# Kernel tuning notes

Hardware: AMD Instinct MI355X
Metric: run time of the kernel (lower is better)

## Reference

```python
import jax, jax.numpy as jnp
import numpy as np
import math

H = 512
V = 64
N = 128
L = 256
T = 20  # min(max_letters, word_tensor.shape[-1])


def _lstm_cell(x, h, c, Wih, Whh, bih, bhh):
    # PyTorch gate order: i, f, g, o
    gates = x @ Wih.T + h @ Whh.T + bih + bhh  # (N, 4H)
    i, f, g, o = jnp.split(gates, 4, axis=-1)
    c_new = jax.nn.sigmoid(f) * c + jax.nn.sigmoid(i) * jnp.tanh(g)
    h_new = jax.nn.sigmoid(o) * jnp.tanh(c_new)
    return h_new, c_new


def setup_inputs() -> dict:
    k = jax.random.key(0)
    ks = jax.random.split(k, 16)
    s = 0.05  # keep activations in a sane range
    return {
        "key": jax.random.normal(ks[0], (N, L, H), jnp.float32),
        "value": jax.random.normal(ks[1], (N, L, H), jnp.float32),
        "encoder_hidden": jax.random.normal(ks[2], (2, N, H), jnp.float32),
        "encoder_cell": jax.random.normal(ks[3], (2, N, H), jnp.float32),
        "word_tensor": jax.random.randint(ks[4], (N, T), 0, V, jnp.int64),
        "embedding": jax.random.normal(ks[5], (V, H), jnp.float32) * s,
        "W_ih0": jax.random.normal(ks[6], (4 * H, 2 * H), jnp.float32) * s,
        "W_hh0": jax.random.normal(ks[7], (4 * H, H), jnp.float32) * s,
        "b_ih0": jax.random.normal(ks[8], (4 * H,), jnp.float32) * s,
        "b_hh0": jax.random.normal(ks[9], (4 * H,), jnp.float32) * s,
        "W_ih1": jax.random.normal(ks[10], (4 * H, H), jnp.float32) * s,
        "W_hh1": jax.random.normal(ks[11], (4 * H, H), jnp.float32) * s,
        "b_ih1": jax.random.normal(ks[12], (4 * H,), jnp.float32) * s,
        "b_hh1": jax.random.normal(ks[13], (4 * H,), jnp.float32) * s,
        "fc_w": jax.random.normal(ks[14], (V, H), jnp.float32) * s,
        "fc_b": jax.random.normal(ks[15], (V,), jnp.float32) * s,
    }


def reference(key, value, encoder_hidden, encoder_cell, word_tensor,
              embedding, W_ih0, W_hh0, b_ih0, b_hh0,
              W_ih1, W_hh1, b_ih1, b_hh1, fc_w, fc_b):
    scale = 1.0 / math.sqrt(H)
    # force_ratio=1.0 -> always teacher-force: inputs are [SOS=0, word[:, :-1]]
    tokens = jnp.concatenate(
        [jnp.zeros((word_tensor.shape[0], 1), word_tensor.dtype),
         word_tensor[:, : T - 1]], axis=1)  # (N, T)
    tokens_t = tokens.T  # (T, N)

    def step(carry, tok):
        h, c = carry  # each (2, N, H)
        emb = embedding[tok]  # (N, H)
        q = h[-1]  # query from top-layer hidden, (N, H)
        scores = jnp.einsum('nh,nlh->nl', q, key) * scale
        attn = jax.nn.softmax(scores, axis=-1)
        ctx = jnp.einsum('nl,nlh->nh', attn, value)  # (N, H)
        x = jnp.concatenate([emb, ctx], axis=-1)  # (N, 2H)
        h0, c0 = _lstm_cell(x, h[0], c[0], W_ih0, W_hh0, b_ih0, b_hh0)
        h1, c1 = _lstm_cell(h0, h[1], c[1], W_ih1, W_hh1, b_ih1, b_hh1)
        logits = h1 @ fc_w.T + fc_b  # (N, V)
        return (jnp.stack([h0, h1]), jnp.stack([c0, c1])), logits

    (h_fin, c_fin), logits_t = jax.lax.scan(step, (encoder_hidden, encoder_cell), tokens_t)
    logits = jnp.transpose(logits_t, (1, 0, 2))  # (N, T, V)
    probs = jax.nn.softmax(logits, axis=-1)
    return probs, h_fin, c_fin
```

## Files before the change

kernel.cpp:

```cpp
#include <hip/hip_runtime.h>
#include <math.h>


#define HH 512
#define VV 64
#define NN 128
#define LL 256
#define TT 20
#define FH 2048
#define LKP 136
#define CSP 36

typedef __attribute__((ext_vector_type(8))) short bf16x8;
typedef __attribute__((ext_vector_type(4))) float f32x4;

__device__ __forceinline__ float sigf(float x) { return 1.0f / (1.0f + expf(-x)); }

__device__ __forceinline__ float wred_max(float x) {
#pragma unroll
  for (int o = 32; o > 0; o >>= 1) x = fmaxf(x, __shfl_xor(x, o));
  return x;
}
__device__ __forceinline__ float wred_sum(float x) {
#pragma unroll
  for (int o = 32; o > 0; o >>= 1) x += __shfl_xor(x, o);
  return x;
}

__global__ __launch_bounds__(256) void k_init(const float* __restrict__ eh,
                                              const float* __restrict__ ec,
                                              float* __restrict__ h0,
                                              float* __restrict__ h1,
                                              float* __restrict__ cfin) {
  int i = blockIdx.x * 256 + threadIdx.x;
  const int NH4 = NN * HH / 4;
  float4 v = ((const float4*)eh)[i];
  if (i < NH4) ((float4*)h0)[i] = v;
  else         ((float4*)h1)[i - NH4] = v;
  ((float4*)cfin)[i] = ((const float4*)ec)[i];
}

__global__ __launch_bounds__(256) void k_pre(const float* __restrict__ emb,
                                             const float* __restrict__ Wih0,
                                             const float* __restrict__ bih0,
                                             const float* __restrict__ bhh0,
                                             float* __restrict__ G) {
  int v = threadIdx.x & 63, jj = threadIdx.x >> 6;
  int j = blockIdx.x * 4 + jj;
  const float4* e4 = (const float4*)(emb + (size_t)v * HH);
  const float4* w4 = (const float4*)(Wih0 + (size_t)j * (2 * HH));
  float acc = 0.f;
#pragma unroll 8
  for (int k = 0; k < HH / 4; ++k) {
    float4 a = e4[k], b = w4[k];
    acc += a.x * b.x + a.y * b.y + a.z * b.z + a.w * b.w;
  }
  G[(size_t)v * FH + ((j & 511) << 2) + (j >> 9)] = acc + bih0[j] + bhh0[j];
}

template <bool DO_FC>
__global__ __launch_bounds__(256) void k_attn2(
    const float* __restrict__ key, const float* __restrict__ value,
    const float* __restrict__ h1cur,
    const float* __restrict__ fc_w, const float* __restrict__ fc_b,
    float* __restrict__ probs, int tprev,
    float* __restrict__ ctxp, float* __restrict__ ms) {
  __shared__ float qs[HH];
  __shared__ float scp[2][128];
  __shared__ float att[128];
  __shared__ float lg[VV];
  __shared__ float red[4];
  int b = blockIdx.x, n = b >> 1, half = b & 1, tid = threadIdx.x;
  ((float2*)qs)[tid] = ((const float2*)(h1cur + (size_t)n * HH))[tid];
  __syncthreads();

  if (DO_FC && half == 0) {
    int v = tid >> 2, p = tid & 3;
    const float4* wr = (const float4*)(fc_w + (size_t)v * HH + p * 128);
    const float4* q4 = (const float4*)(qs + p * 128);
    float a = 0.f;
#pragma unroll 8
    for (int k = 0; k < 32; ++k) {
      float4 w = wr[k], q = q4[k];
      a += w.x * q.x + w.y * q.y + w.z * q.z + w.w * q.w;
    }
    a += __shfl_xor(a, 1);
    a += __shfl_xor(a, 2);
    if (p == 0) lg[v] = a + fc_b[v];
    __syncthreads();
    if (tid < VV) {
      float x = lg[tid];
      float m = wred_max(x);
      float e = expf(x - m);
      float s = wred_sum(e);
      probs[((size_t)n * TT + tprev) * VV + tid] = e / s;
    }
  }

  const float SCALE = 0.044194173824159216f;
  int ll = tid & 127, p = tid >> 7;
  {
    const float4* kr =
        (const float4*)(key + ((size_t)n * LL + half * 128 + ll) * HH + p * 256);
    const float4* q4 = (const float4*)(qs + p * 256);
    float a = 0.f;
#pragma unroll 8
    for (int k = 0; k < 64; ++k) {
      float4 w = kr[k], q = q4[k];
      a += w.x * q.x + w.y * q.y + w.z * q.z + w.w * q.w;
    }
    scp[p][ll] = a;
  }
  __syncthreads();

  float x = 0.f;
  if (tid < 128) {
    x = (scp[0][tid] + scp[1][tid]) * SCALE;
    float m = wred_max(x);
    if ((tid & 63) == 0) red[tid >> 6] = m;
  }
  __syncthreads();
  float m_p = fmaxf(red[0], red[1]);
  if (tid < 128) {
    float e = expf(x - m_p);
    att[tid] = e;
    float s = wred_sum(e);
    if ((tid & 63) == 0) red[2 + (tid >> 6)] = s;
  }
  __syncthreads();
  if (tid == 0) {
    float2 v2 = {m_p, red[2] + red[3]};
    *(float2*)(ms + ((size_t)half * NN + n) * 2) = v2;
  }

  const float* vb = value + ((size_t)n * LL + half * 128) * HH + 2 * tid;
  float cx = 0.f, cy = 0.f;
#pragma unroll 4
  for (int l2 = 0; l2 < 128; ++l2) {
    float a2 = att[l2];
    float2 v2 = *(const float2*)(vb + (size_t)l2 * HH);
    cx += a2 * v2.x;
    cy += a2 * v2.y;
  }
  float2 o2 = {cx, cy};
  ((float2*)(ctxp + ((size_t)half * NN + n) * HH))[tid] = o2;
}

__global__ __launch_bounds__(256) void k_final(
    const float* __restrict__ h1cur, const float* __restrict__ h0cur,
    const float* __restrict__ fc_w, const float* __restrict__ fc_b,
    float* __restrict__ probs, float* __restrict__ hfin) {
  __shared__ float qs[HH];
  __shared__ float lg[VV];
  int n = blockIdx.x, tid = threadIdx.x;
  ((float2*)qs)[tid] = ((const float2*)(h1cur + (size_t)n * HH))[tid];
  ((float2*)(hfin + (size_t)n * HH))[tid] =
      ((const float2*)(h0cur + (size_t)n * HH))[tid];
  ((float2*)(hfin + (size_t)(NN + n) * HH))[tid] =
      ((const float2*)(h1cur + (size_t)n * HH))[tid];
  __syncthreads();
  int v = tid >> 2, p = tid & 3;
  const float4* wr = (const float4*)(fc_w + (size_t)v * HH + p * 128);
  const float4* q4 = (const float4*)(qs + p * 128);
  float a = 0.f;
#pragma unroll 8
  for (int k = 0; k < 32; ++k) {
    float4 w = wr[k], q = q4[k];
    a += w.x * q.x + w.y * q.y + w.z * q.z + w.w * q.w;
  }
  a += __shfl_xor(a, 1);
  a += __shfl_xor(a, 2);
  if (p == 0) lg[v] = a + fc_b[v];
  __syncthreads();
  if (tid < VV) {
    float x = lg[tid];
    float m = wred_max(x);
    float e = expf(x - m);
    float s = wred_sum(e);
    probs[((size_t)n * TT + TT - 1) * VV + tid] = e / s;
  }
}

template <int COMBINE>
__global__ __launch_bounds__(256) void k_gemm(
    const float* __restrict__ Ax0, const float* __restrict__ Ax1,
    const float* __restrict__ Ahh,
    const float* __restrict__ W0, int ws0,
    const float* __restrict__ W1, int ws1,
    const int* __restrict__ word, const float* __restrict__ G,
    const float* __restrict__ bih, const float* __restrict__ bhh,
    const float* __restrict__ ms,
    float* __restrict__ cbuf, float* __restrict__ hnext, int t) {
  __shared__ __align__(16) unsigned short AhS[32 * LKP];
  __shared__ __align__(16) unsigned short AlS[32 * LKP];
  __shared__ __align__(16) unsigned short WhS[32 * LKP];
  __shared__ __align__(16) unsigned short WlS[32 * LKP];
  __shared__ float sc0s[32], sc1s[32];
  __shared__ __align__(16) float Cs[32 * CSP];

  int tid = threadIdx.x;
  int mt = blockIdx.x & 3, nt = blockIdx.x >> 2;
  int s0 = mt * 32, n0 = nt * 32;

  int r = tid >> 3, kq = tid & 7, kk = kq * 16;
  int rowp = n0 + r;
  int jrow = (rowp & 3) * 512 + (rowp >> 2);

  if (COMBINE && tid < 32) {
    int n = s0 + tid;
    float m0 = ms[2 * n], sa = ms[2 * n + 1];
    float m1 = ms[2 * (NN + n)], sb = ms[2 * (NN + n) + 1];
    float m = fmaxf(m0, m1);
    float e0 = expf(m0 - m), e1 = expf(m1 - m);
    float S = sa * e0 + sb * e1;
    sc0s[tid] = e0 / S;
    sc1s[tid] = e1 / S;
  }

  float4 aR0[4], aR1[4], wRg[4];

  auto LOADC = [&](int c) {
    int k0 = c * 128;
    if (k0 < 512) {
      const float4* p0 = (const float4*)(Ax0 + (size_t)(s0 + r) * HH + k0 + kk);
#pragma unroll
      for (int i = 0; i < 4; ++i) aR0[i] = p0[i];
      if (COMBINE) {
        const float4* p1 = (const float4*)(Ax1 + (size_t)(s0 + r) * HH + k0 + kk);
#pragma unroll
        for (int i = 0; i < 4; ++i) aR1[i] = p1[i];
      }
      const float4* wp = (const float4*)(W0 + (size_t)jrow * ws0 + k0 + kk);
#pragma unroll
      for (int i = 0; i < 4; ++i) wRg[i] = wp[i];
    } else {
      const float4* p0 =
          (const float4*)(Ahh + (size_t)(s0 + r) * HH + (k0 - 512) + kk);
#pragma unroll
      for (int i = 0; i < 4; ++i) aR0[i] = p0[i];
      const float4* wp = (const float4*)(W1 + (size_t)jrow * ws1 + (k0 - 512) + kk);
#pragma unroll
      for (int i = 0; i < 4; ++i) wRg[i] = wp[i];
    }
  };

  auto STOREC = [&](int c) {
    int k0 = c * 128;
    bool cmb = COMBINE && (k0 < 512);
    float sa = cmb ? sc0s[r] : 0.f, sb = cmb ? sc1s[r] : 0.f;
#pragma unroll
    for (int i = 0; i < 2; ++i) {
      float xa[8], xw[8];
      float4 u0 = aR0[2 * i], u1 = aR0[2 * i + 1];
      xa[0] = u0.x; xa[1] = u0.y; xa[2] = u0.z; xa[3] = u0.w;
      xa[4] = u1.x; xa[5] = u1.y; xa[6] = u1.z; xa[7] = u1.w;
      if (cmb) {
        float4 v0 = aR1[2 * i], v1 = aR1[2 * i + 1];
        xa[0] = sa * xa[0] + sb * v0.x; xa[1] = sa * xa[1] + sb * v0.y;
        xa[2] = sa * xa[2] + sb * v0.z; xa[3] = sa * xa[3] + sb * v0.w;
        xa[4] = sa * xa[4] + sb * v1.x; xa[5] = sa * xa[5] + sb * v1.y;
        xa[6] = sa * xa[6] + sb * v1.z; xa[7] = sa * xa[7] + sb * v1.w;
      }
      float4 w0 = wRg[2 * i], w1 = wRg[2 * i + 1];
      xw[0] = w0.x; xw[1] = w0.y; xw[2] = w0.z; xw[3] = w0.w;
      xw[4] = w1.x; xw[5] = w1.y; xw[6] = w1.z; xw[7] = w1.w;
      bf16x8 ah, al, wh, wl;
#pragma unroll
      for (int j = 0; j < 8; ++j) {
        unsigned int u = __float_as_uint(xa[j]);
        unsigned int hb = (u + 0x7FFFu + ((u >> 16) & 1u)) & 0xFFFF0000u;
        ah[j] = (short)(hb >> 16);
        float lo = xa[j] - __uint_as_float(hb);
        unsigned int ul = __float_as_uint(lo);
        al[j] = (short)((ul + 0x7FFFu + ((ul >> 16) & 1u)) >> 16);
        u = __float_as_uint(xw[j]);
        hb = (u + 0x7FFFu + ((u >> 16) & 1u)) & 0xFFFF0000u;
        wh[j] = (short)(hb >> 16);
        lo = xw[j] - __uint_as_float(hb);
        ul = __float_as_uint(lo);
        wl[j] = (short)((ul + 0x7FFFu + ((ul >> 16) & 1u)) >> 16);
      }
      int off = r * LKP + kk + i * 8;
      *(bf16x8*)(AhS + off) = ah;
      *(bf16x8*)(AlS + off) = al;
      *(bf16x8*)(WhS + off) = wh;
      *(bf16x8*)(WlS + off) = wl;
    }
  };

  f32x4 acc0 = {0.f, 0.f, 0.f, 0.f};
  f32x4 acc1 = {0.f, 0.f, 0.f, 0.f};
  f32x4 acc2 = {0.f, 0.f, 0.f, 0.f};
  int lane = tid & 63, wv = tid >> 6;
  int wm = wv >> 1, wn = wv & 1;
  int aoff = (wm * 16 + (lane & 15)) * LKP;
  int woff = (wn * 16 + (lane & 15)) * LKP;
  int kb = (lane >> 4) * 8;

  LOADC(0);
  __syncthreads();
  for (int c = 0; c < 8; ++c) {
    if (c) __syncthreads();
    STOREC(c);
    __syncthreads();
    if (c < 7) LOADC(c + 1);
#pragma unroll
    for (int ks = 0; ks < 4; ++ks) {
      int ko = kb + ks * 32;
      bf16x8 ah = *(const bf16x8*)(AhS + aoff + ko);
      bf16x8 al = *(const bf16x8*)(AlS + aoff + ko);
      bf16x8 wh = *(const bf16x8*)(WhS + woff + ko);
      bf16x8 wl = *(const bf16x8*)(WlS + woff + ko);
      acc0 = __builtin_amdgcn_mfma_f32_16x16x32_bf16(ah, wh, acc0, 0, 0, 0);
      acc1 = __builtin_amdgcn_mfma_f32_16x16x32_bf16(al, wh, acc1, 0, 0, 0);
      acc2 = __builtin_amdgcn_mfma_f32_16x16x32_bf16(ah, wl, acc2, 0, 0, 0);
    }
  }

  __syncthreads();
  f32x4 cv = acc0 + acc1;
  cv = cv + acc2;
  int crow = wm * 16 + (lane >> 4) * 4, ccol = wn * 16 + (lane & 15);
#pragma unroll
  for (int q = 0; q < 4; ++q) Cs[(crow + q) * CSP + ccol] = cv[q];
  __syncthreads();
  int s_l = tid >> 3, jh_l = tid & 7;
  int s = s0 + s_l, jh = nt * 8 + jh_l;
  f32x4 c4 = *(const f32x4*)(Cs + s_l * CSP + jh_l * 4);
  if (COMBINE) {
    int tok = (t == 0) ? 0 : (word[s * TT + t - 1] & 63);
    f32x4 g4 = *(const f32x4*)(G + (size_t)tok * FH + jh * 4);
    c4 = c4 + g4;
  } else {
    c4[0] += bih[jh] + bhh[jh];
    c4[1] += bih[512 + jh] + bhh[512 + jh];
    c4[2] += bih[1024 + jh] + bhh[1024 + jh];
    c4[3] += bih[1536 + jh] + bhh[1536 + jh];
  }
  float c_old = cbuf[(size_t)s * HH + jh];
  float cn = sigf(c4[1]) * c_old + sigf(c4[0]) * tanhf(c4[2]);
  cbuf[(size_t)s * HH + jh] = cn;
  hnext[(size_t)s * HH + jh] = sigf(c4[3]) * tanhf(cn);
}

extern "C" void kernel_launch(void* const* d_in, const int* in_sizes, int n_in,
                              void* d_out, int out_size, void* d_ws, size_t ws_size,
                              hipStream_t stream) {
  const float* key   = (const float*)d_in[0];
  const float* value = (const float*)d_in[1];
  const float* eh    = (const float*)d_in[2];
  const float* ec    = (const float*)d_in[3];
  const int*   word  = (const int*)d_in[4];
  const float* emb   = (const float*)d_in[5];
  const float* Wih0  = (const float*)d_in[6];
  const float* Whh0  = (const float*)d_in[7];
  const float* bih0  = (const float*)d_in[8];
  const float* bhh0  = (const float*)d_in[9];
  const float* Wih1  = (const float*)d_in[10];
  const float* Whh1  = (const float*)d_in[11];
  const float* bih1  = (const float*)d_in[12];
  const float* bhh1  = (const float*)d_in[13];
  const float* fcw   = (const float*)d_in[14];
  const float* fcb   = (const float*)d_in[15];

  float* out   = (float*)d_out;
  float* probs = out;
  float* hfin  = out + (size_t)NN * TT * VV;
  float* cfin  = hfin + 2 * (size_t)NN * HH;

  float* ws   = (float*)d_ws;
  float* G    = ws;
  float* ctxp = G + (size_t)VV * FH;
  float* ms   = ctxp + 2 * (size_t)NN * HH;
  float* h0a  = ms + 2 * (size_t)NN * 2;
  float* h0b  = h0a + (size_t)NN * HH;
  float* h1a  = h0b + (size_t)NN * HH;
  float* h1b  = h1a + (size_t)NN * HH;

  k_init<<<128, 256, 0, stream>>>(eh, ec, h0a, h1a, cfin);
  k_pre<<<512, 256, 0, stream>>>(emb, Wih0, bih0, bhh0, G);

  float* h0c = h0a; float* h0n = h0b;
  float* h1c = h1a; float* h1n = h1b;

  for (int t = 0; t < TT; ++t) {
    if (t == 0)
      k_attn2<false><<<256, 256, 0, stream>>>(key, value, h1c, fcw, fcb,
                                              probs, 0, ctxp, ms);
    else
      k_attn2<true><<<256, 256, 0, stream>>>(key, value, h1c, fcw, fcb,
                                             probs, t - 1, ctxp, ms);

    k_gemm<1><<<256, 256, 0, stream>>>(
        ctxp, ctxp + (size_t)NN * HH, h0c, Wih0 + 512, 2 * HH, Whh0, HH,
        word, G, bih0, bhh0, ms, cfin, h0n, t);
    k_gemm<0><<<256, 256, 0, stream>>>(
        h0n, (const float*)nullptr, h1c, Wih1, HH, Whh1, HH,
        word, G, bih1, bhh1, ms, cfin + (size_t)NN * HH, h1n, t);

    float* tmp;
    tmp = h0c; h0c = h0n; h0n = tmp;
    tmp = h1c; h1c = h1n; h1n = tmp;
  }

  k_final<<<128, 256, 0, stream>>>(h1c, h0c, fcw, fcb, probs, hfin);
}
```

Before: 1.310 ms.

## Convert key/value to bf16 once and split attention into score and context kernels

Adds one-time kernels that convert key to bf16 and value to a transposed bf16 layout. Each step's attention then becomes two kernels: a score kernel with per-32-chunk softmax partials, and a context kernel that merges the partials and reads the transposed value. This halves the per-step key/value bytes, which are read 20 times, and raises block count for parallelism. The cost is an extra launch per step, bf16 rounding error in the attention, and an upfront conversion pass; the old path is kept as a fallback when the workspace is too small.

```diff
diff --git a/kernel.cpp b/kernel.cpp
--- a/kernel.cpp
+++ b/kernel.cpp
@@ -15,6 +15,13 @@
 typedef __attribute__((ext_vector_type(4))) float f32x4;
 
 __device__ __forceinline__ float sigf(float x) { return 1.0f / (1.0f + expf(-x)); }
+__device__ __forceinline__ unsigned short f2bf(float x) {
+  unsigned int u = __float_as_uint(x);
+  return (unsigned short)((u + 0x7FFFu + ((u >> 16) & 1u)) >> 16);
+}
+__device__ __forceinline__ float bf2f(short b) {
+  return __uint_as_float(((unsigned int)(unsigned short)b) << 16);
+}
 
 __device__ __forceinline__ float wred_max(float x) {
 #pragma unroll
@@ -26,6 +33,7 @@
   for (int o = 32; o > 0; o >>= 1) x += __shfl_xor(x, o);
   return x;
 }
+
 
 __global__ __launch_bounds__(256) void k_init(const float* __restrict__ eh,
                                               const float* __restrict__ ec,
@@ -58,6 +66,216 @@
   G[(size_t)v * FH + ((j & 511) << 2) + (j >> 9)] = acc + bih0[j] + bhh0[j];
 }
 
+__global__ __launch_bounds__(256) void k_prepK(const float* __restrict__ K,
+                                               unsigned short* __restrict__ Kb) {
+  size_t i = ((size_t)blockIdx.x * 256 + threadIdx.x) * 8;
+  float4 a = *(const float4*)(K + i);
+  float4 b = *(const float4*)(K + i + 4);
+  bf16x8 o;
+  o[0] = f2bf(a.x); o[1] = f2bf(a.y); o[2] = f2bf(a.z); o[3] = f2bf(a.w);
+  o[4] = f2bf(b.x); o[5] = f2bf(b.y); o[6] = f2bf(b.z); o[7] = f2bf(b.w);
+  *(bf16x8*)(Kb + i) = o;
+}
+
+__global__ __launch_bounds__(256) void k_prepVt(const float* __restrict__ V,
+                                                unsigned short* __restrict__ Vt) {
+  __shared__ float tile[64 * 65];
+  int bx = blockIdx.x;
+  int n = bx >> 5, lt = (bx >> 3) & 3, ht = bx & 7;
+  int l0 = lt * 64, h0 = ht * 64;
+  int tid = threadIdx.x;
+  int r = tid >> 2, c = (tid & 3) * 16;
+  const float4* src = (const float4*)(V + ((size_t)n * LL + l0 + r) * HH + h0 + c);
+#pragma unroll
+  for (int j = 0; j < 4; ++j) {
+    float4 u = src[j];
+    tile[r * 65 + c + j * 4 + 0] = u.x;
+    tile[r * 65 + c + j * 4 + 1] = u.y;
+    tile[r * 65 + c + j * 4 + 2] = u.z;
+    tile[r * 65 + c + j * 4 + 3] = u.w;
+  }
+  __syncthreads();
+  int hrow = tid >> 2, lcol = (tid & 3) * 16;
+  bf16x8 o0, o1;
+#pragma unroll
+  for (int j = 0; j < 8; ++j) o0[j] = f2bf(tile[(lcol + j) * 65 + hrow]);
+#pragma unroll
+  for (int j = 0; j < 8; ++j) o1[j] = f2bf(tile[(lcol + 8 + j) * 65 + hrow]);
+  bf16x8* dst = (bf16x8*)(Vt + ((size_t)n * HH + h0 + hrow) * LL + l0 + lcol);
+  dst[0] = o0;
+  dst[1] = o1;
+}
+
+
+#define ASCALE 0.044194173824159216f
+
+__global__ __launch_bounds__(256) void k_score(
+    const unsigned short* __restrict__ Kb, const float* __restrict__ h1cur,
+    float* __restrict__ sc, float* __restrict__ msb) {
+  __shared__ float qs[HH];
+  __shared__ float srow[32];
+  int bx = blockIdx.x, tid = threadIdx.x;
+  int n = bx >> 3, lq = bx & 7;
+  ((float2*)qs)[tid] = ((const float2*)(h1cur + (size_t)n * HH))[tid];
+  __syncthreads();
+  int row = tid >> 3, p = tid & 7;
+  const bf16x8* kr =
+      (const bf16x8*)(Kb + ((size_t)n * LL + lq * 32 + row) * HH + p * 64);
+  float a = 0.f;
+#pragma unroll
+  for (int i = 0; i < 8; ++i) {
+    bf16x8 kv = kr[i];
+    const float* q8 = qs + p * 64 + i * 8;
+#pragma unroll
+    for (int j = 0; j < 8; ++j) a += bf2f(kv[j]) * q8[j];
+  }
+  a += __shfl_xor(a, 1);
+  a += __shfl_xor(a, 2);
+  a += __shfl_xor(a, 4);
+  if (p == 0) srow[row] = a * ASCALE;
+  __syncthreads();
+  if (tid < 32) {
+    float x = srow[tid];
+    float m = x;
+#pragma unroll
+    for (int o = 16; o > 0; o >>= 1) m = fmaxf(m, __shfl_xor(m, o));
+    float e = expf(x - m);
+    float s = e;
+#pragma unroll
+    for (int o = 16; o > 0; o >>= 1) s += __shfl_xor(s, o);
+    sc[(size_t)n * LL + lq * 32 + tid] = e;
+    if (tid == 0) {
+      float2 v2 = {m, s};
+      *(float2*)(msb + ((size_t)lq * NN + n) * 2) = v2;
+    }
+  }
+}
+
+template <bool DO_FC>
+__global__ __launch_bounds__(256) void k_ctx(
+    const unsigned short* __restrict__ Vt, const float* __restrict__ sc,
+    const float* __restrict__ msb, float* __restrict__ ctx,
+    const float* __restrict__ h1cur, const float* __restrict__ fc_w,
+    const float* __restrict__ fc_b, float* __restrict__ probs, int tprev) {
+  __shared__ float att[LL];
+  __shared__ float redP[128];
+  __shared__ float hs[8 * HH];
+  int bx = blockIdx.x, tid = threadIdx.x;
+
+  if (DO_FC && bx >= 512) {
+    int n0 = (bx - 512) * 8;
+#pragma unroll
+    for (int i = 0; i < 4; ++i) {
+      int fi = tid + i * 256;
+      int r = fi >> 7, k4 = fi & 127;
+      ((float4*)hs)[r * 128 + k4] =
+          ((const float4*)(h1cur + (size_t)(n0 + r) * HH))[k4];
+    }
+    __syncthreads();
+    int nl = tid >> 5, vb = (tid & 31) * 2;
+    const float4* h4 = (const float4*)(hs + nl * HH);
+    const float4* w0 = (const float4*)(fc_w + (size_t)vb * HH);
+    const float4* w1 = (const float4*)(fc_w + (size_t)(vb + 1) * HH);
+    float a0 = 0.f, a1 = 0.f;
+#pragma unroll 8
+    for (int k = 0; k < 128; ++k) {
+      float4 h = h4[k], x0 = w0[k], x1 = w1[k];
+      a0 += h.x * x0.x + h.y * x0.y + h.z * x0.z + h.w * x0.w;
+      a1 += h.x * x1.x + h.y * x1.y + h.z * x1.z + h.w * x1.w;
+    }
+    a0 += fc_b[vb];
+    a1 += fc_b[vb + 1];
+    float m = fmaxf(a0, a1);
+#pragma unroll
+    for (int o = 16; o > 0; o >>= 1) m = fmaxf(m, __shfl_xor(m, o));
+    float e0 = expf(a0 - m), e1 = expf(a1 - m);
+    float s = e0 + e1;
+#pragma unroll
+    for (int o = 16; o > 0; o >>= 1) s += __shfl_xor(s, o);
+    float inv = 1.f / s;
+    float2 pr = {e0 * inv, e1 * inv};
+    *(float2*)(probs + ((size_t)(n0 + nl) * TT + tprev) * VV + vb) = pr;
+    return;
+  }
+
+  int n = bx >> 2, ht = bx & 3;
+  int hl = tid & 127, lg = tid >> 7;
+  float mp[8], sp[8];
+#pragma unroll
+  for (int i = 0; i < 8; ++i) {
+    float2 v2 = *(const float2*)(msb + ((size_t)i * NN + n) * 2);
+    mp[i] = v2.x;
+    sp[i] = v2.y;
+  }
+  float m = mp[0];
+#pragma unroll
+  for (int i = 1; i < 8; ++i) m = fmaxf(m, mp[i]);
+  float S = 0.f;
+#pragma unroll
+  for (int i = 0; i < 8; ++i) {
+    mp[i] = expf(mp[i] - m);
+    S += sp[i] * mp[i];
+  }
+  float invS = 1.f / S;
+  {
+    int l = tid;
+    att[l] = sc[(size_t)n * LL + l] * mp[l >> 5] * invS;
+  }
+  __syncthreads();
+
+  int h = ht * 128 + hl;
+  const bf16x8* vt =
+      (const bf16x8*)(Vt + ((size_t)n * HH + h) * LL + lg * 128);
+  const float* ab = att + lg * 128;
+  float acc = 0.f;
+#pragma unroll
+  for (int i = 0; i < 16; ++i) {
+    bf16x8 v8 = vt[i];
+    const float* a8 = ab + i * 8;
+#pragma unroll
+    for (int j = 0; j < 8; ++j) acc += bf2f(v8[j]) * a8[j];
+  }
+  if (lg == 1) redP[hl] = acc;
+  __syncthreads();
+  if (lg == 0) ctx[(size_t)n * HH + h] = acc + redP[hl];
+}
+
+__global__ __launch_bounds__(256) void k_final(
+    const float* __restrict__ h1cur, const float* __restrict__ h0cur,
+    const float* __restrict__ fc_w, const float* __restrict__ fc_b,
+    float* __restrict__ probs, float* __restrict__ hfin) {
+  __shared__ float qs[HH];
+  __shared__ float lg[VV];
+  int n = blockIdx.x, tid = threadIdx.x;
+  ((float2*)qs)[tid] = ((const float2*)(h1cur + (size_t)n * HH))[tid];
+  ((float2*)(hfin + (size_t)n * HH))[tid] =
+      ((const float2*)(h0cur + (size_t)n * HH))[tid];
+  ((float2*)(hfin + (size_t)(NN + n) * HH))[tid] =
+      ((const float2*)(h1cur + (size_t)n * HH))[tid];
+  __syncthreads();
+  int v = tid >> 2, p = tid & 3;
+  const float4* wr = (const float4*)(fc_w + (size_t)v * HH + p * 128);
+  const float4* q4 = (const float4*)(qs + p * 128);
+  float a = 0.f;
+#pragma unroll 8
+  for (int k = 0; k < 32; ++k) {
+    float4 w = wr[k], q = q4[k];
+    a += w.x * q.x + w.y * q.y + w.z * q.z + w.w * q.w;
+  }
+  a += __shfl_xor(a, 1);
+  a += __shfl_xor(a, 2);
+  if (p == 0) lg[v] = a + fc_b[v];
+  __syncthreads();
+  if (tid < VV) {
+    float x = lg[tid];
+    float m = wred_max(x);
+    float e = expf(x - m);
+    float s = wred_sum(e);
+    probs[((size_t)n * TT + TT - 1) * VV + tid] = e / s;
+  }
+}
+
+
 template <bool DO_FC>
 __global__ __launch_bounds__(256) void k_attn2(
     const float* __restrict__ key, const float* __restrict__ value,
@@ -97,7 +315,6 @@
     }
   }
 
-  const float SCALE = 0.044194173824159216f;
   int ll = tid & 127, p = tid >> 7;
   {
     const float4* kr =
@@ -115,7 +332,7 @@
 
   float x = 0.f;
   if (tid < 128) {
-    x = (scp[0][tid] + scp[1][tid]) * SCALE;
+    x = (scp[0][tid] + scp[1][tid]) * ASCALE;
     float m = wred_max(x);
     if ((tid & 63) == 0) red[tid >> 6] = m;
   }
@@ -146,42 +363,7 @@
   ((float2*)(ctxp + ((size_t)half * NN + n) * HH))[tid] = o2;
 }
 
-__global__ __launch_bounds__(256) void k_final(
-    const float* __restrict__ h1cur, const float* __restrict__ h0cur,
-    const float* __restrict__ fc_w, const float* __restrict__ fc_b,
-    float* __restrict__ probs, float* __restrict__ hfin) {
-  __shared__ float qs[HH];
-  __shared__ float lg[VV];
-  int n = blockIdx.x, tid = threadIdx.x;
-  ((float2*)qs)[tid] = ((const float2*)(h1cur + (size_t)n * HH))[tid];
-  ((float2*)(hfin + (size_t)n * HH))[tid] =
-      ((const float2*)(h0cur + (size_t)n * HH))[tid];
-  ((float2*)(hfin + (size_t)(NN + n) * HH))[tid] =
-      ((const float2*)(h1cur + (size_t)n * HH))[tid];
-  __syncthreads();
-  int v = tid >> 2, p = tid & 3;
-  const float4* wr = (const float4*)(fc_w + (size_t)v * HH + p * 128);
-  const float4* q4 = (const float4*)(qs + p * 128);
-  float a = 0.f;
-#pragma unroll 8
-  for (int k = 0; k < 32; ++k) {
-    float4 w = wr[k], q = q4[k];
-    a += w.x * q.x + w.y * q.y + w.z * q.z + w.w * q.w;
-  }
-  a += __shfl_xor(a, 1);
-  a += __shfl_xor(a, 2);
-  if (p == 0) lg[v] = a + fc_b[v];
-  __syncthreads();
-  if (tid < VV) {
-    float x = lg[tid];
-    float m = wred_max(x);
-    float e = expf(x - m);
-    float s = wred_sum(e);
-    probs[((size_t)n * TT + TT - 1) * VV + tid] = e / s;
-  }
-}
-
-template <int COMBINE>
+template <int MODE>
 __global__ __launch_bounds__(256) void k_gemm(
     const float* __restrict__ Ax0, const float* __restrict__ Ax1,
     const float* __restrict__ Ahh,
@@ -206,7 +388,7 @@
   int rowp = n0 + r;
   int jrow = (rowp & 3) * 512 + (rowp >> 2);
 
-  if (COMBINE && tid < 32) {
+  if (MODE == 2 && tid < 32) {
     int n = s0 + tid;
     float m0 = ms[2 * n], sa = ms[2 * n + 1];
     float m1 = ms[2 * (NN + n)], sb = ms[2 * (NN + n) + 1];
@@ -225,7 +407,7 @@
       const float4* p0 = (const float4*)(Ax0 + (size_t)(s0 + r) * HH + k0 + kk);
 #pragma unroll
       for (int i = 0; i < 4; ++i) aR0[i] = p0[i];
-      if (COMBINE) {
+      if (MODE == 2) {
         const float4* p1 = (const float4*)(Ax1 + (size_t)(s0 + r) * HH + k0 + kk);
 #pragma unroll
         for (int i = 0; i < 4; ++i) aR1[i] = p1[i];
@@ -246,7 +428,7 @@
 
   auto STOREC = [&](int c) {
     int k0 = c * 128;
-    bool cmb = COMBINE && (k0 < 512);
+    bool cmb = (MODE == 2) && (k0 < 512);
     float sa = cmb ? sc0s[r] : 0.f, sb = cmb ? sc1s[r] : 0.f;
 #pragma unroll
     for (int i = 0; i < 2; ++i) {
@@ -271,14 +453,12 @@
         unsigned int hb = (u + 0x7FFFu + ((u >> 16) & 1u)) & 0xFFFF0000u;
         ah[j] = (short)(hb >> 16);
         float lo = xa[j] - __uint_as_float(hb);
-        unsigned int ul = __float_as_uint(lo);
-        al[j] = (short)((ul + 0x7FFFu + ((ul >> 16) & 1u)) >> 16);
+        al[j] = (short)f2bf(lo);
         u = __float_as_uint(xw[j]);
         hb = (u + 0x7FFFu + ((u >> 16) & 1u)) & 0xFFFF0000u;
         wh[j] = (short)(hb >> 16);
         lo = xw[j] - __uint_as_float(hb);
-        ul = __float_as_uint(lo);
-        wl[j] = (short)((ul + 0x7FFFu + ((ul >> 16) & 1u)) >> 16);
+        wl[j] = (short)f2bf(lo);
       }
       int off = r * LKP + kk + i * 8;
       *(bf16x8*)(AhS + off) = ah;
@@ -327,7 +507,7 @@
   int s_l = tid >> 3, jh_l = tid & 7;
   int s = s0 + s_l, jh = nt * 8 + jh_l;
   f32x4 c4 = *(const f32x4*)(Cs + s_l * CSP + jh_l * 4);
-  if (COMBINE) {
+  if (MODE >= 1) {
     int tok = (t == 0) ? 0 : (word[s * TT + t - 1] & 63);
     f32x4 g4 = *(const f32x4*)(G + (size_t)tok * FH + jh * 4);
     c4 = c4 + g4;
@@ -342,6 +522,7 @@
   cbuf[(size_t)s * HH + jh] = cn;
   hnext[(size_t)s * HH + jh] = sigf(c4[3]) * tanhf(cn);
 }
+
 
 extern "C" void kernel_launch(void* const* d_in, const int* in_sizes, int n_in,
                               void* d_out, int out_size, void* d_ws, size_t ws_size,
@@ -368,14 +549,19 @@
   float* hfin  = out + (size_t)NN * TT * VV;
   float* cfin  = hfin + 2 * (size_t)NN * HH;
 
-  float* ws   = (float*)d_ws;
+  float* ws = (float*)d_ws;
   float* G    = ws;
-  float* ctxp = G + (size_t)VV * FH;
-  float* ms   = ctxp + 2 * (size_t)NN * HH;
-  float* h0a  = ms + 2 * (size_t)NN * 2;
-  float* h0b  = h0a + (size_t)NN * HH;
-  float* h1a  = h0b + (size_t)NN * HH;
-  float* h1b  = h1a + (size_t)NN * HH;
+  float* ctx  = G + 131072;
+  float* h0a  = ctx + 65536;
+  float* h0b  = h0a + 65536;
+  float* h1a  = h0b + 65536;
+  float* h1b  = h1a + 65536;
+  float* sc   = h1b + 65536;
+  float* msb  = sc + 32768;
+  unsigned short* Kb = (unsigned short*)(msb + 4096);
+  unsigned short* Vt = Kb + (size_t)NN * LL * HH;
+  const size_t NEED = ((size_t)131072 + 65536 * 5 + 32768 + 4096) * 4 +
+                      (size_t)2 * NN * LL * HH * 2;
 
   k_init<<<128, 256, 0, stream>>>(eh, ec, h0a, h1a, cfin);
   k_pre<<<512, 256, 0, stream>>>(emb, Wih0, bih0, bhh0, G);
@@ -383,24 +569,56 @@
   float* h0c = h0a; float* h0n = h0b;
   float* h1c = h1a; float* h1n = h1b;
 
-  for (int t = 0; t < TT; ++t) {
-    if (t == 0)
-      k_attn2<false><<<256, 256, 0, stream>>>(key, value, h1c, fcw, fcb,
-                                              probs, 0, ctxp, ms);
-    else
-      k_attn2<true><<<256, 256, 0, stream>>>(key, value, h1c, fcw, fcb,
-                                             probs, t - 1, ctxp, ms);
-
-    k_gemm<1><<<256, 256, 0, stream>>>(
-        ctxp, ctxp + (size_t)NN * HH, h0c, Wih0 + 512, 2 * HH, Whh0, HH,
-        word, G, bih0, bhh0, ms, cfin, h0n, t);
-    k_gemm<0><<<256, 256, 0, stream>>>(
-        h0n, (const float*)nullptr, h1c, Wih1, HH, Whh1, HH,
-        word, G, bih1, bhh1, ms, cfin + (size_t)NN * HH, h1n, t);
-
-    float* tmp;
-    tmp = h0c; h0c = h0n; h0n = tmp;
-    tmp = h1c; h1c = h1n; h1n = tmp;
+  if (ws_size >= NEED) {
+    k_prepK<<<8192, 256, 0, stream>>>(key, Kb);
+    k_prepVt<<<4096, 256, 0, stream>>>(value, Vt);
+
+    for (int t = 0; t < TT; ++t) {
+      k_score<<<1024, 256, 0, stream>>>(Kb, h1c, sc, msb);
+      if (t == 0)
+        k_ctx<false><<<512, 256, 0, stream>>>(Vt, sc, msb, ctx, h1c, fcw, fcb,
+                                              probs, 0);
+      else
+        k_ctx<true><<<528, 256, 0, stream>>>(Vt, sc, msb, ctx, h1c, fcw, fcb,
+                                             probs, t - 1);
+      k_gemm<1><<<256, 256, 0, stream>>>(
+          ctx, (const float*)nullptr, h0c, Wih0 + 512, 2 * HH, Whh0, HH,
+          word, G, bih0, bhh0, (const float*)nullptr, cfin, h0n, t);
+      k_gemm<0><<<256, 256, 0, stream>>>(
+          h0n, (const float*)nullptr, h1c, Wih1, HH, Whh1, HH,
+          word, G, bih1, bhh1, (const float*)nullptr,
+          cfin + (size_t)NN * HH, h1n, t);
+      float* tmp;
+      tmp = h0c; h0c = h0n; h0n = tmp;
+      tmp = h1c; h1c = h1n; h1n = tmp;
+    }
+  } else {
+    float* ctxp = G + 131072;
+    float* ms2 = ctxp + 131072;
+    float* f0a = ms2 + 512;
+    float* f0b = f0a + 65536;
+    float* f1a = f0b + 65536;
+    float* f1b = f1a + 65536;
+    k_init<<<128, 256, 0, stream>>>(eh, ec, f0a, f1a, cfin);
+    h0c = f0a; h0n = f0b; h1c = f1a; h1n = f1b;
+    for (int t = 0; t < TT; ++t) {
+      if (t == 0)
+        k_attn2<false><<<256, 256, 0, stream>>>(key, value, h1c, fcw, fcb,
+                                                probs, 0, ctxp, ms2);
+      else
+        k_attn2<true><<<256, 256, 0, stream>>>(key, value, h1c, fcw, fcb,
+                                               probs, t - 1, ctxp, ms2);
+      k_gemm<2><<<256, 256, 0, stream>>>(
+          ctxp, ctxp + (size_t)NN * HH, h0c, Wih0 + 512, 2 * HH, Whh0, HH,
+          word, G, bih0, bhh0, ms2, cfin, h0n, t);
+      k_gemm<0><<<256, 256, 0, stream>>>(
+          h0n, (const float*)nullptr, h1c, Wih1, HH, Whh1, HH,
+          word, G, bih1, bhh1, (const float*)nullptr,
+          cfin + (size_t)NN * HH, h1n, t);
+      float* tmp;
+      tmp = h0c; h0c = h0n; h0n = tmp;
+      tmp = h1c; h1c = h1n; h1n = tmp;
+    }
   }
 
   k_final<<<128, 256, 0, stream>>>(h1c, h0c, fcw, fcb, probs, hfin);
```

New measurement: 1.719 ms. +31.3%, slower.
